# Performance work log

Measured on AMD Instinct MI355X. Metric: run time of the kernel, lower is better.

Reference implementation:

```python
import jax, jax.numpy as jnp
import numpy as np

B, C, H, W = 8, 256, 96, 96
GH, GW = 16, 16                # proto_grid
KH, KW = H // GH, W // GW      # avg-pool kernel = stride
P = GH * GW                    # local prototypes per sample
THRESH = 0.95
NORM_EPS = 1e-4


def _safe_norm(x, axis):
    # L2-normalize with norm clamped below at NORM_EPS (matches safe_norm)
    n = jnp.sqrt(jnp.sum(x * x, axis=axis, keepdims=True))
    return x / jnp.maximum(n, NORM_EPS)


def _avg_pool(x):
    # [B, c, H, W] -> [B, c, P] non-overlapping KHxKW average pooling
    b, c = x.shape[:2]
    return x.reshape(b, c, GH, KH, GW, KW).mean(axis=(3, 5)).reshape(b, c, P)


def setup_inputs() -> dict:
    key = jax.random.key(0)
    k1, k2, k3, k4 = jax.random.split(key, 4)
    qry_fts = jax.random.normal(k1, (B, C, H, W), dtype=jnp.float32)
    sup_fts = jax.random.normal(k2, (B, C, H, W), dtype=jnp.float32)
    sup_mask = (jax.random.uniform(k3, (B, 1, H, W)) > 0.02).astype(jnp.float32)
    true_bg_mask = (jax.random.uniform(k4, (B, 1, H, W)) > 0.9).astype(jnp.float32)
    return {"qry_fts": qry_fts, "sup_fts": sup_fts,
            "sup_mask": sup_mask, "true_bg_mask": true_bg_mask}


def reference(qry_fts, sup_fts, sup_mask, true_bg_mask):
    # mode='gridconv+' path, vectorized: ragged prototype selection -> masked softmax
    local_fts = _avg_pool(sup_fts).transpose(0, 2, 1)       # [B, P, C]
    local_mask = _avg_pool(sup_mask)[:, 0, :]               # [B, P]
    local_bg = _avg_pool(true_bg_mask)[:, 0, :]             # [B, P]
    valid = (local_mask > THRESH) & (local_bg < 0.5)        # [B, P] bool

    # global masked-average prototype
    gproto = jnp.sum(sup_fts * sup_mask, axis=(-1, -2)) / (
        jnp.sum(sup_mask, axis=(-1, -2)) + 1e-5)            # [B, C]

    protos = jnp.concatenate([local_fts, gproto[:, None, :]], axis=1)  # [B, P+1, C]
    valid_all = jnp.concatenate(
        [valid, jnp.ones((B, 1), dtype=bool)], axis=1)      # global always valid

    protos_n = _safe_norm(protos, axis=2)                   # [B, P+1, C]
    qry_n = _safe_norm(qry_fts, axis=1)                     # [B, C, H, W]

    # 1x1 conv with prototype weights == batched cosine similarity
    dists = jnp.einsum('bchw,bpc->bphw', qry_n, protos_n)   # [B, P+1, H, W]

    # softmax restricted to valid prototypes (invalid get weight 0)
    logits = jnp.where(valid_all[:, :, None, None], dists, -jnp.inf)
    w = jax.nn.softmax(logits, axis=1)
    pred = jnp.sum(w * dists, axis=1, keepdims=True)        # [B, 1, H, W]
    return pred
```

## Files before the change

kernel.cpp:

```cpp
#include <hip/hip_runtime.h>

#define BB 8
#define CC 256
#define HH 96
#define WW 96
#define HWW (HH*WW)
#define NLOC 256
#define PPAD 257
#define THRESH 0.95f
#define NORM_EPS 1e-4f

typedef __attribute__((ext_vector_type(8))) _Float16 f16x8;
typedef __attribute__((ext_vector_type(16))) float f32x16;

union H16 { _Float16 f; unsigned short u; };

__global__ void k01(const float* __restrict__ sup_fts,
                    const float* __restrict__ sup_mask,
                    const float* __restrict__ true_bg,
                    float* __restrict__ protos,
                    float* __restrict__ validf,
                    float* __restrict__ masksum) {
    __shared__ float red[256];
    int blk = blockIdx.x;
    int t = threadIdx.x;
    if (blk < BB * CC) {
        int b = blk >> 8, c = blk & 255;
        int gy = t >> 4, gx = t & 15;
        const float* fb = sup_fts + ((size_t)b * CC + c) * HWW;
        const float* mb = sup_mask + (size_t)b * HWW;
        int base = gy * 6 * WW + gx * 6;
        float fs = 0.f, fm = 0.f;
        for (int r = 0; r < 6; ++r) {
            const float* rowf = fb + base + r * WW;
            const float* rowm = mb + base + r * WW;
#pragma unroll
            for (int h = 0; h < 3; ++h) {
                float2 v  = *(const float2*)(rowf + 2 * h);
                float2 mk = *(const float2*)(rowm + 2 * h);
                fs += v.x + v.y;
                fm = fmaf(v.x, mk.x, fm);
                fm = fmaf(v.y, mk.y, fm);
            }
        }
        protos[((size_t)b * PPAD + t) * CC + c] = fs * (1.f / 36.f);
        red[t] = fm;
        __syncthreads();
        for (int off = 128; off > 0; off >>= 1) {
            if (t < off) red[t] += red[t + off];
            __syncthreads();
        }
        if (t == 0) protos[((size_t)b * PPAD + 256) * CC + c] = red[0];
    } else {
        int b = blk - BB * CC;
        int gy = t >> 4, gx = t & 15;
        const float* mb = sup_mask + (size_t)b * HWW;
        const float* gb = true_bg  + (size_t)b * HWW;
        int base = gy * 6 * WW + gx * 6;
        float ms = 0.f, bs = 0.f;
        for (int r = 0; r < 6; ++r) {
            const float* rowm = mb + base + r * WW;
            const float* rowg = gb + base + r * WW;
#pragma unroll
            for (int h = 0; h < 3; ++h) {
                float2 mk = *(const float2*)(rowm + 2 * h);
                float2 bg2 = *(const float2*)(rowg + 2 * h);
                ms += mk.x + mk.y;
                bs += bg2.x + bg2.y;
            }
        }
        float mmean = ms * (1.f / 36.f);
        float bmean = bs * (1.f / 36.f);
        validf[b * PPAD + t] = (mmean > THRESH && bmean < 0.5f) ? 1.f : 0.f;
        if (t == 0) validf[b * PPAD + 256] = 1.f;
        red[t] = ms;
        __syncthreads();
        for (int off = 128; off > 0; off >>= 1) {
            if (t < off) red[t] += red[t + off];
            __syncthreads();
        }
        if (t == 0) masksum[b] = red[0];
    }
}

__global__ void k2_norm(float* __restrict__ protos,
                        const float* __restrict__ masksum,
                        unsigned short* __restrict__ Pimg) {
    int bp = blockIdx.x;
    int b = bp / PPAD;
    int p = bp - b * PPAD;
    int t = threadIdx.x;
    float v = protos[((size_t)b * PPAD + p) * CC + t];
    if (p == 256) v = v / (masksum[b] + 1e-5f);
    __shared__ float red[256];
    red[t] = v * v;
    __syncthreads();
    for (int off = 128; off > 0; off >>= 1) {
        if (t < off) red[t] += red[t + off];
        __syncthreads();
    }
    float norm = sqrtf(red[0]);
    float vn = v / fmaxf(norm, NORM_EPS);
    protos[((size_t)b * PPAD + p) * CC + t] = vn;
    if (p < NLOC) {
        H16 h; h.f = (_Float16)vn;
        int kstep = t >> 4, khalf = (t >> 3) & 1, e = t & 7;
        int tile = p >> 5, col = p & 31;
        size_t idx = ((((size_t)b * 16 + kstep) * 2 + khalf) * 8 + tile) * 256
                     + col * 8 + e;
        Pimg[idx] = h.u;
    }
}

__global__ __launch_bounds__(256, 4)
void k3_mfma(const float* __restrict__ qry,
             const unsigned short* __restrict__ Pimg,
             const float* __restrict__ protos_n,
             const float* __restrict__ validf,
             float* __restrict__ out) {
    __shared__ alignas(16) float Qraw[256 * 32];
    __shared__ float gpl[256];
    __shared__ float rn_s[32], gd_s[32];
    __shared__ float S_l[4][32], N_l[4][32];

    int blk = blockIdx.x;
    int b = blk & 7;
    int tpx = blk >> 3;
    int px0 = tpx * 32;
    int t = threadIdx.x;
    int l = t & 63;
    int w = t >> 6;
    int col = l & 31;
    int h = l >> 5;

    const float* qbase = qry + (size_t)b * CC * HWW;
    const float* gp = protos_n + ((size_t)b * PPAD + 256) * CC;
    const unsigned short* Pb = Pimg + (size_t)b * 65536;

    float vf0 = validf[b * PPAD + w * 64 + col];
    float vf1 = validf[b * PPAD + w * 64 + 32 + col];

    gpl[t] = gp[t];
    {
        char* dstbase = (char*)Qraw + w * 1024;
#pragma unroll
        for (int i = 0; i < 8; ++i) {
            int F = i * 256 + t;
            int ch = F >> 3, pxq = F & 7;
            __builtin_amdgcn_global_load_lds(
                (const void*)(qbase + (size_t)ch * HWW + px0 + pxq * 4),
                (void*)(dstbase + i * 4096), 16, 0, 0);
        }
    }
    __syncthreads();

    f32x16 acc[2];
#pragma unroll
    for (int i = 0; i < 16; ++i) { acc[0][i] = 0.f; acc[1][i] = 0.f; }
    f16x8 Bf[2][2];
    float nrm = 0.f, gac = 0.f;

#define LOADB(KS, BUF)                                                        \
    {                                                                         \
        _Pragma("unroll")                                                     \
        for (int ti = 0; ti < 2; ++ti)                                        \
            Bf[BUF][ti] = *(const f16x8*)(Pb +                                \
                ((((size_t)(KS) * 2 + h) * 8 + (w * 2 + ti)) * 32 + col) * 8);\
    }

    LOADB(0, 0);
    LOADB(1, 1);

#pragma unroll
    for (int ks = 0; ks < 16; ++ks) {
        int c0 = ks * 16 + h * 8;
        float qv[8];
#pragma unroll
        for (int i = 0; i < 8; ++i) qv[i] = Qraw[(c0 + i) * 32 + col];
        unsigned int us[8];
#pragma unroll
        for (int i = 0; i < 8; ++i) {
            H16 x; x.f = (_Float16)qv[i];
            us[i] = x.u;
            nrm = fmaf(qv[i], qv[i], nrm);
            gac = fmaf(qv[i], gpl[c0 + i], gac);
        }
        union { f16x8 v; unsigned int u[4]; } QA;
        QA.u[0] = us[0] | (us[1] << 16); QA.u[1] = us[2] | (us[3] << 16);
        QA.u[2] = us[4] | (us[5] << 16); QA.u[3] = us[6] | (us[7] << 16);
#pragma unroll
        for (int ti = 0; ti < 2; ++ti)
            acc[ti] = __builtin_amdgcn_mfma_f32_32x32x16_f16(QA.v, Bf[ks & 1][ti], acc[ti], 0, 0, 0);
        if (ks + 2 < 16) LOADB(ks + 2, ks & 1);
    }
#undef LOADB

    nrm += __shfl_xor(nrm, 32);
    gac += __shfl_xor(gac, 32);
    if (w == 0 && l < 32) {
        float rn = 1.f / fmaxf(sqrtf(nrm), NORM_EPS);
        rn_s[l] = rn;
        gd_s[l] = gac * rn;
    }
    __syncthreads();

#pragma unroll
    for (int r = 0; r < 16; ++r) {
        int row = (r & 3) + 8 * (r >> 2) + 4 * h;
        float rnv = rn_s[row];
        float d0 = acc[0][r] * rnv;
        float d1 = acc[1][r] * rnv;
        float l0 = (vf0 != 0.f) ? d0 : -1e30f;
        float l1 = (vf1 != 0.f) ? d1 : -1e30f;
        float e0 = __expf(l0 - 1.1f);
        float e1 = __expf(l1 - 1.1f);
        float s = e0 + e1;
        float nn = fmaf(e0, l0, e1 * l1);
#pragma unroll
        for (int m = 1; m < 32; m <<= 1) {
            s  += __shfl_xor(s, m);
            nn += __shfl_xor(nn, m);
        }
        if (col == 0) { S_l[w][row] = s; N_l[w][row] = nn; }
    }
    __syncthreads();

    if (t < 32) {
        float gdv = gd_s[t];
        float eg = __expf(gdv - 1.1f);
        float S = eg, N = eg * gdv;
#pragma unroll
        for (int i = 0; i < 4; ++i) { S += S_l[i][t]; N += N_l[i][t]; }
        out[(size_t)b * HWW + px0 + t] = N / S;
    }
}

extern "C" void kernel_launch(void* const* d_in, const int* in_sizes, int n_in,
                              void* d_out, int out_size, void* d_ws, size_t ws_size,
                              hipStream_t stream) {
    const float* qry = (const float*)d_in[0];
    const float* sup = (const float*)d_in[1];
    const float* msk = (const float*)d_in[2];
    const float* bg  = (const float*)d_in[3];
    float* out = (float*)d_out;

    float* ws = (float*)d_ws;
    float* protos  = ws;
    float* validf  = protos + (size_t)BB * PPAD * CC;
    float* masksum = validf + (size_t)BB * PPAD;
    unsigned short* Pimg = (unsigned short*)(masksum + BB);

    hipLaunchKernelGGL(k01, dim3(BB * CC + BB), dim3(256), 0, stream,
                       sup, msk, bg, protos, validf, masksum);
    hipLaunchKernelGGL(k2_norm, dim3(BB * PPAD), dim3(256), 0, stream, protos, masksum, Pimg);
    hipLaunchKernelGGL(k3_mfma, dim3(BB * (HWW / 32)), dim3(256), 0, stream,
                       qry, Pimg, protos, validf, out);
}
```

Baseline: 64.70 us.

## Process two pixel tiles per block with double-buffered LDS prefetch

Each k3 block now computes two consecutive 32-pixel tiles, using a second LDS buffer. The query slice for the second tile is loaded while the first tile's MFMA loop and softmax run, hiding global load latency behind compute. The grid is halved and launch bounds are lowered to 2 blocks per CU because LDS use doubles. This trades away occupancy and adds an extra barrier per tile.

```diff
diff --git a/kernel.cpp b/kernel.cpp
--- a/kernel.cpp
+++ b/kernel.cpp
@@ -112,21 +112,21 @@
     }
 }
 
-__global__ __launch_bounds__(256, 4)
+__global__ __launch_bounds__(256, 2)
 void k3_mfma(const float* __restrict__ qry,
              const unsigned short* __restrict__ Pimg,
              const float* __restrict__ protos_n,
              const float* __restrict__ validf,
              float* __restrict__ out) {
-    __shared__ alignas(16) float Qraw[256 * 32];
+    __shared__ alignas(16) float Qraw[2][256 * 32];
     __shared__ float gpl[256];
     __shared__ float rn_s[32], gd_s[32];
     __shared__ float S_l[4][32], N_l[4][32];
 
-    int blk = blockIdx.x;
-    int b = blk & 7;
-    int tpx = blk >> 3;
-    int px0 = tpx * 32;
+    int bid = blockIdx.x;
+    int b = bid & 7;
+    int tgrp = bid >> 3;
+    int px0 = tgrp * 64;
     int t = threadIdx.x;
     int l = t & 63;
     int w = t >> 6;
@@ -140,25 +140,18 @@
     float vf0 = validf[b * PPAD + w * 64 + col];
     float vf1 = validf[b * PPAD + w * 64 + 32 + col];
 
-    gpl[t] = gp[t];
-    {
-        char* dstbase = (char*)Qraw + w * 1024;
-#pragma unroll
-        for (int i = 0; i < 8; ++i) {
-            int F = i * 256 + t;
-            int ch = F >> 3, pxq = F & 7;
-            __builtin_amdgcn_global_load_lds(
-                (const void*)(qbase + (size_t)ch * HWW + px0 + pxq * 4),
-                (void*)(dstbase + i * 4096), 16, 0, 0);
-        }
-    }
-    __syncthreads();
-
-    f32x16 acc[2];
-#pragma unroll
-    for (int i = 0; i < 16; ++i) { acc[0][i] = 0.f; acc[1][i] = 0.f; }
-    f16x8 Bf[2][2];
-    float nrm = 0.f, gac = 0.f;
+#define STAGE(PX0, BUF)                                                       \
+    {                                                                         \
+        char* dstbase = (char*)&Qraw[BUF][0] + w * 1024;                      \
+        _Pragma("unroll")                                                     \
+        for (int i = 0; i < 8; ++i) {                                         \
+            int F = i * 256 + t;                       \
+            int ch = F >> 3, pxq = F & 7;                                     \
+            __builtin_amdgcn_global_load_lds(                                 \
+                (const void*)(qbase + (size_t)ch * HWW + (PX0) + pxq * 4),    \
+                (void*)(dstbase + i * 4096), 16, 0, 0);                       \
+        }                                                                     \
+    }
 
 #define LOADB(KS, BUF)                                                        \
     {                                                                         \
@@ -168,71 +161,88 @@
                 ((((size_t)(KS) * 2 + h) * 8 + (w * 2 + ti)) * 32 + col) * 8);\
     }
 
-    LOADB(0, 0);
-    LOADB(1, 1);
-
-#pragma unroll
-    for (int ks = 0; ks < 16; ++ks) {
-        int c0 = ks * 16 + h * 8;
-        float qv[8];
-#pragma unroll
-        for (int i = 0; i < 8; ++i) qv[i] = Qraw[(c0 + i) * 32 + col];
-        unsigned int us[8];
-#pragma unroll
-        for (int i = 0; i < 8; ++i) {
-            H16 x; x.f = (_Float16)qv[i];
-            us[i] = x.u;
-            nrm = fmaf(qv[i], qv[i], nrm);
-            gac = fmaf(qv[i], gpl[c0 + i], gac);
-        }
-        union { f16x8 v; unsigned int u[4]; } QA;
-        QA.u[0] = us[0] | (us[1] << 16); QA.u[1] = us[2] | (us[3] << 16);
-        QA.u[2] = us[4] | (us[5] << 16); QA.u[3] = us[6] | (us[7] << 16);
-#pragma unroll
-        for (int ti = 0; ti < 2; ++ti)
-            acc[ti] = __builtin_amdgcn_mfma_f32_32x32x16_f16(QA.v, Bf[ks & 1][ti], acc[ti], 0, 0, 0);
-        if (ks + 2 < 16) LOADB(ks + 2, ks & 1);
-    }
+    gpl[t] = gp[t];
+    STAGE(px0, 0);
+    __syncthreads();
+
+#pragma unroll
+    for (int tix2 = 0; tix2 < 2; ++tix2) {
+        if (tix2 == 0) STAGE(px0 + 32, 1);
+
+        f32x16 acc[2];
+#pragma unroll
+        for (int i = 0; i < 16; ++i) { acc[0][i] = 0.f; acc[1][i] = 0.f; }
+        f16x8 Bf[2][2];
+        float nrm = 0.f, gac = 0.f;
+        const float* Qb = &Qraw[tix2][0];
+
+        LOADB(0, 0);
+        LOADB(1, 1);
+#pragma unroll
+        for (int ks = 0; ks < 16; ++ks) {
+            int c0 = ks * 16 + h * 8;
+            float qv[8];
+#pragma unroll
+            for (int i = 0; i < 8; ++i) qv[i] = Qb[(c0 + i) * 32 + col];
+            unsigned int us[8];
+#pragma unroll
+            for (int i = 0; i < 8; ++i) {
+                H16 x; x.f = (_Float16)qv[i];
+                us[i] = x.u;
+                nrm = fmaf(qv[i], qv[i], nrm);
+                gac = fmaf(qv[i], gpl[c0 + i], gac);
+            }
+            union { f16x8 v; unsigned int u[4]; } QA;
+            QA.u[0] = us[0] | (us[1] << 16); QA.u[1] = us[2] | (us[3] << 16);
+            QA.u[2] = us[4] | (us[5] << 16); QA.u[3] = us[6] | (us[7] << 16);
+#pragma unroll
+            for (int ti = 0; ti < 2; ++ti)
+                acc[ti] = __builtin_amdgcn_mfma_f32_32x32x16_f16(QA.v, Bf[ks & 1][ti], acc[ti], 0, 0, 0);
+            if (ks + 2 < 16) LOADB(ks + 2, ks & 1);
+        }
+
+        nrm += __shfl_xor(nrm, 32);
+        gac += __shfl_xor(gac, 32);
+        if (w == 0 && l < 32) {
+            float rn = 1.f / fmaxf(sqrtf(nrm), NORM_EPS);
+            rn_s[l] = rn;
+            gd_s[l] = gac * rn;
+        }
+        __syncthreads();
+
+#pragma unroll
+        for (int r = 0; r < 16; ++r) {
+            int row = (r & 3) + 8 * (r >> 2) + 4 * h;
+            float rnv = rn_s[row];
+            float d0 = acc[0][r] * rnv;
+            float d1 = acc[1][r] * rnv;
+            float l0 = (vf0 != 0.f) ? d0 : -1e30f;
+            float l1 = (vf1 != 0.f) ? d1 : -1e30f;
+            float e0 = __expf(l0 - 1.1f);
+            float e1 = __expf(l1 - 1.1f);
+            float s = e0 + e1;
+            float nn = fmaf(e0, l0, e1 * l1);
+#pragma unroll
+            for (int m = 1; m < 32; m <<= 1) {
+                s  += __shfl_xor(s, m);
+                nn += __shfl_xor(nn, m);
+            }
+            if (col == 0) { S_l[w][row] = s; N_l[w][row] = nn; }
+        }
+        __syncthreads();
+
+        if (t < 32) {
+            float gdv = gd_s[t];
+            float eg = __expf(gdv - 1.1f);
+            float S = eg, N = eg * gdv;
+#pragma unroll
+            for (int i = 0; i < 4; ++i) { S += S_l[i][t]; N += N_l[i][t]; }
+            out[(size_t)b * HWW + px0 + tix2 * 32 + t] = N / S;
+        }
+        if (tix2 == 0) __syncthreads();
+    }
+#undef STAGE
 #undef LOADB
-
-    nrm += __shfl_xor(nrm, 32);
-    gac += __shfl_xor(gac, 32);
-    if (w == 0 && l < 32) {
-        float rn = 1.f / fmaxf(sqrtf(nrm), NORM_EPS);
-        rn_s[l] = rn;
-        gd_s[l] = gac * rn;
-    }
-    __syncthreads();
-
-#pragma unroll
-    for (int r = 0; r < 16; ++r) {
-        int row = (r & 3) + 8 * (r >> 2) + 4 * h;
-        float rnv = rn_s[row];
-        float d0 = acc[0][r] * rnv;
-        float d1 = acc[1][r] * rnv;
-        float l0 = (vf0 != 0.f) ? d0 : -1e30f;
-        float l1 = (vf1 != 0.f) ? d1 : -1e30f;
-        float e0 = __expf(l0 - 1.1f);
-        float e1 = __expf(l1 - 1.1f);
-        float s = e0 + e1;
-        float nn = fmaf(e0, l0, e1 * l1);
-#pragma unroll
-        for (int m = 1; m < 32; m <<= 1) {
-            s  += __shfl_xor(s, m);
-            nn += __shfl_xor(nn, m);
-        }
-        if (col == 0) { S_l[w][row] = s; N_l[w][row] = nn; }
-    }
-    __syncthreads();
-
-    if (t < 32) {
-        float gdv = gd_s[t];
-        float eg = __expf(gdv - 1.1f);
-        float S = eg, N = eg * gdv;
-#pragma unroll
-        for (int i = 0; i < 4; ++i) { S += S_l[i][t]; N += N_l[i][t]; }
-        out[(size_t)b * HWW + px0 + t] = N / S;
-    }
 }
 
 extern "C" void kernel_launch(void* const* d_in, const int* in_sizes, int n_in,
@@ -253,6 +263,6 @@
     hipLaunchKernelGGL(k01, dim3(BB * CC + BB), dim3(256), 0, stream,
                        sup, msk, bg, protos, validf, masksum);
     hipLaunchKernelGGL(k2_norm, dim3(BB * PPAD), dim3(256), 0, stream, protos, masksum, Pimg);
-    hipLaunchKernelGGL(k3_mfma, dim3(BB * (HWW / 32)), dim3(256), 0, stream,
+    hipLaunchKernelGGL(k3_mfma, dim3(BB * (HWW / 64)), dim3(256), 0, stream,
                        qry, Pimg, protos, validf, out);
 }
```

After: 80.37 us. 1.24x slower.
